# Kernel optimization log

Measured on AMD Instinct MI355X. Metric: run time of the kernel, lower is better.

Reference implementation:

```python
import math
import jax, jax.numpy as jnp
import numpy as np

DIM = 1536; NH = 12; HD = DIM // NH        # head_dim = 128
F, H, W = 4, 20, 26
S = F * H * W                              # 2080 tokens
BLOCK = 128
SPAD = math.ceil(S / BLOCK) * BLOCK        # 2176
EPS = 1e-6
C = HD // 2
SF, SH, SW = C - 2 * (C // 3), C // 3, C // 3   # 22, 21, 21 rotary bands


def _rope_params(max_len, d, theta=10000.0):
    inv = 1.0 / (theta ** (np.arange(0, d, 2, dtype=np.float64) / d))
    return np.outer(np.arange(max_len), inv)   # [max_len, d//2] angles


def _rope(x, freqs, f, h, w):
    # x: [b, s, n, d] with s == f*h*w; freqs: [1024, d//2] angles
    b, s, n, d = x.shape
    ang = jnp.concatenate([
        jnp.broadcast_to(freqs[:f, :SF][:, None, None, :], (f, h, w, SF)),
        jnp.broadcast_to(freqs[:h, SF:SF + SH][None, :, None, :], (f, h, w, SH)),
        jnp.broadcast_to(freqs[:w, SF + SH:C][None, None, :, :], (f, h, w, SW)),
    ], axis=-1).reshape(s, C)
    cos = jnp.cos(ang)[None, :, None, :]
    sin = jnp.sin(ang)[None, :, None, :]
    xr = x.reshape(b, s, n, C, 2)
    x0, x1 = xr[..., 0], xr[..., 1]          # complex mult (x0+ix1)*(cos+isin)
    out = jnp.stack([x0 * cos - x1 * sin, x0 * sin + x1 * cos], axis=-1)
    return out.reshape(b, s, n, d)


def setup_inputs():
    key = jax.random.key(0)
    ks = jax.random.split(key, 6)
    freqs = jnp.asarray(np.concatenate([
        _rope_params(1024, 2 * SF), _rope_params(1024, 2 * SH), _rope_params(1024, 2 * SW)
    ], axis=1), dtype=jnp.float32)           # [1024, 64]
    lin = lambda k: jax.random.normal(k, (DIM, DIM), jnp.float32) * 0.02
    blk = jnp.arange(SPAD) // BLOCK
    # block-causal (128-token blocks) mask, padding keys (>= S) masked out
    mask = (blk[:, None] >= blk[None, :]) & (jnp.arange(SPAD)[None, :] < S)
    return {
        "x": jax.random.normal(ks[0], (1, S, DIM), jnp.float32),
        "freqs": freqs,
        "wq": lin(ks[1]), "bq": jnp.zeros((DIM,), jnp.float32),
        "wk": lin(ks[2]), "bk": jnp.zeros((DIM,), jnp.float32),
        "wv": lin(ks[3]), "bv": jnp.zeros((DIM,), jnp.float32),
        "wo": lin(ks[4]), "bo": jnp.zeros((DIM,), jnp.float32),
        "gq": jnp.ones((DIM,), jnp.float32),
        "gk": jnp.ones((DIM,), jnp.float32),
        "seq_lens": jnp.array([S], jnp.int32),
        "grid_sizes": jnp.array([[F, H, W]], jnp.int32),
        "mask": mask,
    }


def reference(x, freqs, wq, bq, wk, bk, wv, bv, wo, bo, gq, gk, seq_lens, grid_sizes, mask):
    b, s, _ = x.shape
    n, d = NH, HD
    rms = lambda t, g: (t * jax.lax.rsqrt(jnp.mean(t * t, axis=-1, keepdims=True) + EPS)) * g
    q = rms(x @ wq + bq, gq).reshape(b, s, n, d)
    k = rms(x @ wk + bk, gk).reshape(b, s, n, d)
    v = (x @ wv + bv).reshape(b, s, n, d)
    f, h, w = int(grid_sizes[0, 0]), int(grid_sizes[0, 1]), int(grid_sizes[0, 2])
    sl = int(seq_lens[0])
    if sl > 0 and s == 2 * sl:  # teacher forcing: rope each half independently
        q = jnp.concatenate([_rope(q[:, :sl], freqs, f, h, w), _rope(q[:, sl:], freqs, f, h, w)], axis=1)
        k = jnp.concatenate([_rope(k[:, :sl], freqs, f, h, w), _rope(k[:, sl:], freqs, f, h, w)], axis=1)
    else:
        q = _rope(q, freqs, f, h, w)
        k = _rope(k, freqs, f, h, w)
    pad = SPAD - s
    if pad > 0:
        pz = ((0, 0), (0, pad), (0, 0), (0, 0))
        q, k, v = jnp.pad(q, pz), jnp.pad(k, pz), jnp.pad(v, pz)
    scores = jnp.einsum('bqnd,bknd->bnqk', q, k) / math.sqrt(d)
    scores = jnp.where(mask[None, None], scores, -jnp.inf)
    attn = jax.nn.softmax(scores, axis=-1)
    o = jnp.einsum('bnqk,bknd->bqnd', attn, v)[:, :s].reshape(b, s, n * d)
    return o @ wo + bo
```

## Files before the change

### kernel.cpp

```cpp
#include <hip/hip_runtime.h>

#define DIMM   1536
#define NHEAD  12
#define HD     128
#define SEQ    2080
#define SPADN  2176
#define HWPROD 520
#define SCALE  0.08838834764831845f
#define K2F    0.12751744154f

typedef short short8  __attribute__((ext_vector_type(8)));
typedef float floatx4 __attribute__((ext_vector_type(4)));

__device__ __forceinline__ unsigned short f2bf(float f) {
    union { float f; unsigned u; } v; v.f = f;
    return (unsigned short)((v.u + 0x7fffu + ((v.u >> 16) & 1u)) >> 16);
}

__device__ __forceinline__ void gld_lds16(const void* g, void* l) {
    __builtin_amdgcn_global_load_lds(
        (const __attribute__((address_space(1))) unsigned int*)g,
        (__attribute__((address_space(3))) unsigned int*)l, 16, 0, 0);
}

__constant__ int c_base[33] = {0,1,2,3,4,5,6,7,
                               8,10,12,14,16,18,20,22,
                               24,27,30,33,36,39,42,45,
                               48,52,56,60,64,68,72,76,
                               80};
#define SLOTS_PER_HEAD 85

__global__ void k_prep(const float* __restrict__ x,
                       const float* __restrict__ w0, const float* __restrict__ w1,
                       const float* __restrict__ w2, const float* __restrict__ w3,
                       unsigned short* __restrict__ xb,
                       unsigned short* __restrict__ t0, unsigned short* __restrict__ t1,
                       unsigned short* __restrict__ t2, unsigned short* __restrict__ t3) {
    int z = blockIdx.z;
    if (z == 4) {
        int n4 = SEQ * DIMM / 4;
        int idx = (blockIdx.y * 24 + blockIdx.x) * 256 + threadIdx.x;
#pragma unroll
        for (int i = 0; i < 6; i++) {
            int p = idx + i * 147456;
            if (p < n4) {
                float4 v = ((const float4*)x)[p];
                ushort4 o;
                o.x = f2bf(v.x); o.y = f2bf(v.y); o.z = f2bf(v.z); o.w = f2bf(v.w);
                ((ushort4*)xb)[p] = o;
            }
        }
        return;
    }
    const float* in = (z == 0) ? w0 : (z == 1) ? w1 : (z == 2) ? w2 : w3;
    unsigned short* out = (z == 0) ? t0 : (z == 1) ? t1 : (z == 2) ? t2 : t3;
    __shared__ float tile[64][65];
    int tx = threadIdx.x & 63, ty = threadIdx.x >> 6;
    int r0 = blockIdx.x * 64, c0 = blockIdx.y * 64;
#pragma unroll
    for (int i = 0; i < 16; i++)
        tile[i * 4 + ty][tx] = in[(size_t)(r0 + i * 4 + ty) * DIMM + c0 + tx];
    __syncthreads();
#pragma unroll
    for (int i = 0; i < 16; i++) {
        int cc = i * 4 + ty;
        out[(size_t)(c0 + cc) * DIMM + r0 + tx] = f2bf(tile[tx][cc]);
    }
}

__global__ void k_transpose_bf16(const float* __restrict__ in, unsigned short* __restrict__ out,
                                 int Rvalid, int Rout, int C) {
    __shared__ float tile[64][65];
    int tx = threadIdx.x & 63, ty = threadIdx.x >> 6;
    int r0 = blockIdx.x * 64, c0 = blockIdx.y * 64;
#pragma unroll
    for (int i = 0; i < 16; i++) {
        int rr = i * 4 + ty;
        int gr = r0 + rr;
        tile[rr][tx] = (gr < Rvalid) ? in[(size_t)gr * C + c0 + tx] : 0.f;
    }
    __syncthreads();
#pragma unroll
    for (int i = 0; i < 16; i++) {
        int cc = i * 4 + ty;
        out[(size_t)(c0 + cc) * Rout + r0 + tx] = f2bf(tile[tx][cc]);
    }
}

__global__ __launch_bounds__(256, 3) void k_gemm(
    const unsigned short* __restrict__ A,
    const unsigned short* __restrict__ B0, const unsigned short* __restrict__ B1,
    const unsigned short* __restrict__ B2,
    const float* __restrict__ bias0, const float* __restrict__ bias1, const float* __restrict__ bias2,
    float* __restrict__ C0, float* __restrict__ C1, float* __restrict__ C2,
    int M, int N, int K) {
    const unsigned short* B = B0; const float* bias = bias0; float* C = C0;
    if (blockIdx.z == 1) { B = B1; bias = bias1; C = C1; }
    if (blockIdx.z == 2) { B = B2; bias = bias2; C = C2; }

    __shared__ unsigned short As[128 * 64];
    __shared__ unsigned short Bs[128 * 64];

    int tid = threadIdx.x;
    int lane = tid & 63, wv = tid >> 6;
    int quad = lane >> 4, l16 = lane & 15;
    int m0 = blockIdx.y * 128, n0 = blockIdx.x * 128;
    int wm = (wv >> 1) * 64, wn = (wv & 1) * 64;
    int sw = l16 & 7;

    int srow_in_blk = lane >> 3;
    int schunk = lane & 7;
    int gchunk = schunk ^ (srow_in_blk & 7);

    floatx4 acc[4][4];
#pragma unroll
    for (int i = 0; i < 4; i++)
#pragma unroll
        for (int j = 0; j < 4; j++) acc[i][j] = (floatx4){0.f, 0.f, 0.f, 0.f};

    for (int k0 = 0; k0 < K; k0 += 64) {
#pragma unroll
        for (int i = 0; i < 4; i++) {
            int blkrow = (wv * 4 + i) * 8;
            int r = blkrow + srow_in_blk;
            int ra = m0 + r; if (ra > M - 1) ra = M - 1;
            gld_lds16(A + (size_t)ra * K + k0 + gchunk * 8, &As[blkrow * 64]);
            gld_lds16(B + (size_t)(n0 + r) * K + k0 + gchunk * 8, &Bs[blkrow * 64]);
        }
        __syncthreads();
#pragma unroll
        for (int kc = 0; kc < 2; kc++) {
            short8 af[4], bfr[4];
#pragma unroll
            for (int t = 0; t < 4; t++) {
                int ca = ((kc * 4 + quad) ^ sw) << 3;
                af[t]  = *(const short8*)&As[(wm + t * 16 + l16) * 64 + ca];
                bfr[t] = *(const short8*)&Bs[(wn + t * 16 + l16) * 64 + ca];
            }
#pragma unroll
            for (int mi = 0; mi < 4; mi++)
#pragma unroll
                for (int ni = 0; ni < 4; ni++)
                    acc[mi][ni] = __builtin_amdgcn_mfma_f32_16x16x32_bf16(af[mi], bfr[ni], acc[mi][ni], 0, 0, 0);
        }
        __syncthreads();
    }
#pragma unroll
    for (int mi = 0; mi < 4; mi++) {
#pragma unroll
        for (int r = 0; r < 4; r++) {
            int row = m0 + wm + mi * 16 + quad * 4 + r;
            if (row < M) {
#pragma unroll
                for (int ni = 0; ni < 4; ni++) {
                    int col = n0 + wn + ni * 16 + l16;
                    C[(size_t)row * N + col] = acc[mi][ni][r] + bias[col];
                }
            }
        }
    }
}

__global__ __launch_bounds__(256, 8) void k_gemm64(
    const unsigned short* __restrict__ A, const unsigned short* __restrict__ B,
    const float* __restrict__ bias, float* __restrict__ C, int M, int N, int K) {
    __shared__ unsigned short As[64 * 64];
    __shared__ unsigned short Bs[64 * 64];
    int tid = threadIdx.x;
    int lane = tid & 63, wv = tid >> 6;
    int quad = lane >> 4, l16 = lane & 15;
    int m0 = blockIdx.y * 64, n0 = blockIdx.x * 64;
    int wm = (wv >> 1) * 32, wn = (wv & 1) * 32;

    int srow = lane >> 3;
    int schunk = lane & 7;

    floatx4 acc[2][2];
#pragma unroll
    for (int i = 0; i < 2; i++)
#pragma unroll
        for (int j = 0; j < 2; j++) acc[i][j] = (floatx4){0.f, 0.f, 0.f, 0.f};

    for (int k0 = 0; k0 < K; k0 += 64) {
#pragma unroll
        for (int i = 0; i < 2; i++) {
            int rb = (i * 4 + wv) * 8;
            int r = rb + srow;
            int g = schunk ^ (r & 7);
            int ra = m0 + r; if (ra > M - 1) ra = M - 1;
            gld_lds16(A + (size_t)ra * K + k0 + g * 8, &As[rb * 64]);
            gld_lds16(B + (size_t)(n0 + r) * K + k0 + g * 8, &Bs[rb * 64]);
        }
        __syncthreads();
#pragma unroll
        for (int kc = 0; kc < 2; kc++) {
            short8 af[2], bfr[2];
#pragma unroll
            for (int t = 0; t < 2; t++) {
                int rowa = wm + t * 16 + l16;
                int rowb = wn + t * 16 + l16;
                int c = kc * 4 + quad;
                af[t]  = *(const short8*)&As[rowa * 64 + ((c ^ (rowa & 7)) << 3)];
                bfr[t] = *(const short8*)&Bs[rowb * 64 + ((c ^ (rowb & 7)) << 3)];
            }
#pragma unroll
            for (int mi = 0; mi < 2; mi++)
#pragma unroll
                for (int ni = 0; ni < 2; ni++)
                    acc[mi][ni] = __builtin_amdgcn_mfma_f32_16x16x32_bf16(af[mi], bfr[ni], acc[mi][ni], 0, 0, 0);
        }
        __syncthreads();
    }
#pragma unroll
    for (int mi = 0; mi < 2; mi++) {
#pragma unroll
        for (int r = 0; r < 4; r++) {
            int row = m0 + wm + mi * 16 + quad * 4 + r;
            if (row < M) {
#pragma unroll
                for (int ni = 0; ni < 2; ni++) {
                    int col = n0 + wn + ni * 16 + l16;
                    C[(size_t)row * N + col] = acc[mi][ni][r] + bias[col];
                }
            }
        }
    }
}

__global__ void k_rmsrope(const float* __restrict__ Qf, const float* __restrict__ Kf,
                          const float* __restrict__ gq, const float* __restrict__ gk,
                          const float* __restrict__ freqs,
                          unsigned short* __restrict__ Qa, unsigned short* __restrict__ Ka) {
    __shared__ float redq[4], redk[4];
    int s = blockIdx.x;
    int tid = threadIdx.x;
    int lane = tid & 63, wv = tid >> 6;
    const float2* qrow = (const float2*)(Qf + (size_t)s * DIMM);
    const float2* krow = (const float2*)(Kf + (size_t)s * DIMM);
    const float2* g2q = (const float2*)gq;
    const float2* g2k = (const float2*)gk;

    float2 qv[3], kv[3];
    float sq = 0.f, sk = 0.f;
#pragma unroll
    for (int j = 0; j < 3; j++) {
        int p = tid + j * 256;
        qv[j] = qrow[p]; kv[j] = krow[p];
        sq += qv[j].x * qv[j].x + qv[j].y * qv[j].y;
        sk += kv[j].x * kv[j].x + kv[j].y * kv[j].y;
    }
#pragma unroll
    for (int m = 32; m >= 1; m >>= 1) { sq += __shfl_xor(sq, m); sk += __shfl_xor(sk, m); }
    if (lane == 0) { redq[wv] = sq; redk[wv] = sk; }
    __syncthreads();
    float tq = redq[0] + redq[1] + redq[2] + redq[3];
    float tk = redk[0] + redk[1] + redk[2] + redk[3];
    float scq = rsqrtf(tq * (1.f / DIMM) + 1e-6f);
    float sck = rsqrtf(tk * (1.f / DIMM) + 1e-6f);

    int fi = s / HWPROD;
    int rem = s - fi * HWPROD;
    int hi = rem / 26;
    int wi = rem - hi * 26;
#pragma unroll
    for (int j = 0; j < 3; j++) {
        int p = tid + j * 256;
        int c = p & 63;
        int pos = (c < 22) ? fi : ((c < 43) ? hi : wi);
        float ang = freqs[pos * 64 + c];
        float sn, cs;
        __sincosf(ang, &sn, &cs);
        float2 gqa = g2q[p];
        float q0 = qv[j].x * scq * gqa.x, q1 = qv[j].y * scq * gqa.y;
        ushort2 oq; oq.x = f2bf(q0 * cs - q1 * sn); oq.y = f2bf(q0 * sn + q1 * cs);
        float2 gka = g2k[p];
        float kk0 = kv[j].x * sck * gka.x, kk1 = kv[j].y * sck * gka.y;
        ushort2 ok; ok.x = f2bf(kk0 * cs - kk1 * sn); ok.y = f2bf(kk0 * sn + kk1 * cs);
        int h = p >> 6;
        size_t off = ((size_t)h * SPADN + s) * HD + 2 * c;
        *(ushort2*)(Qa + off) = oq;
        *(ushort2*)(Ka + off) = ok;
    }
}

__global__ __launch_bounds__(256, 3) void k_attn1(const unsigned short* __restrict__ Qa,
                                                  const unsigned short* __restrict__ Ka,
                                                  const unsigned short* __restrict__ Vt,
                                                  float* __restrict__ Opart,
                                                  float* __restrict__ Lpart) {
    int j = blockIdx.x, h = blockIdx.y, z = blockIdx.z;
    int nkb = (j >> 1) * 2 + 2;
    if (nkb > 33) nkb = 33;
    int kb0 = z * 8;
    if (kb0 >= nkb) return;
    int kb1 = kb0 + 8; if (kb1 > nkb) kb1 = nkb;

    __shared__ unsigned short Ks[64 * 128];
    __shared__ unsigned short Vs[128 * 64];
    __shared__ unsigned short Ps[4][16][72];

    int tid = threadIdx.x;
    int lane = tid & 63, wv = tid >> 6;
    int quad = lane >> 4, l16 = lane & 15;
    int qrow0 = j * 64 + wv * 16;

    short8 qf[4];
#pragma unroll
    for (int kc = 0; kc < 4; kc++)
        qf[kc] = *(const short8*)(Qa + ((size_t)h * SPADN + qrow0 + l16) * HD + kc * 32 + quad * 8);

    short8 ones8;
#pragma unroll
    for (int i = 0; i < 8; i++) ones8[i] = (short)0x3F80;

    floatx4 of[8], of9;
#pragma unroll
    for (int ni = 0; ni < 8; ni++) of[ni] = (floatx4){0.f, 0.f, 0.f, 0.f};
    of9 = (floatx4){0.f, 0.f, 0.f, 0.f};

    int krow = lane >> 4;
    int kslot = lane & 15;
    int vrow = lane >> 3;
    int vslot = lane & 7;

    for (int kb = kb0; kb < kb1; kb++) {
        const unsigned short* kbase = Ka + (((size_t)h * SPADN + kb * 64) * HD);
#pragma unroll
        for (int i = 0; i < 4; i++) {
            int rb = i * 4 + wv;
            int r = rb * 4 + krow;
            int g = (kslot & 8) | ((kslot & 7) ^ (r & 7));
            gld_lds16(kbase + r * 128 + g * 8, &Ks[rb * 512]);
        }
#pragma unroll
        for (int i = 0; i < 4; i++) {
            int rb = i * 4 + wv;
            int r = rb * 8 + vrow;
            int g = vslot ^ (r & 7);
            gld_lds16(Vt + ((size_t)h * HD + r) * SPADN + kb * 64 + g * 8, &Vs[rb * 512]);
        }
        __syncthreads();

        floatx4 sa[4];
#pragma unroll
        for (int ni = 0; ni < 4; ni++) sa[ni] = (floatx4){0.f, 0.f, 0.f, 0.f};
#pragma unroll
        for (int kc = 0; kc < 4; kc++) {
            int c = kc * 4 + quad;
            short8 kf[4];
#pragma unroll
            for (int ni = 0; ni < 4; ni++) {
                int row = ni * 16 + l16;
                int slot = (c & 8) | ((c & 7) ^ (row & 7));
                kf[ni] = *(const short8*)&Ks[row * 128 + slot * 8];
            }
#pragma unroll
            for (int ni = 0; ni < 4; ni++)
                sa[ni] = __builtin_amdgcn_mfma_f32_16x16x32_bf16(qf[kc], kf[ni], sa[ni], 0, 0, 0);
        }

        bool maskb = (kb == 32);
#pragma unroll
        for (int r = 0; r < 4; r++) {
#pragma unroll
            for (int ni = 0; ni < 4; ni++) {
                float xv = sa[ni][r] * K2F;
                if (maskb && (kb * 64 + ni * 16 + l16 >= SEQ)) xv = -1e30f;
                float p = exp2f(fminf(xv, 36.f));
                Ps[wv][quad * 4 + r][ni * 16 + l16] = f2bf(p);
            }
        }
#pragma unroll
        for (int kc = 0; kc < 2; kc++) {
            int ko = kc * 32 + quad * 8;
            short8 pf = *(const short8*)&Ps[wv][l16][ko];
            int c = kc * 4 + quad;
#pragma unroll
            for (int ni = 0; ni < 8; ni++) {
                int row = ni * 16 + l16;
                short8 vf = *(const short8*)&Vs[row * 64 + ((c ^ (row & 7)) << 3)];
                of[ni] = __builtin_amdgcn_mfma_f32_16x16x32_bf16(pf, vf, of[ni], 0, 0, 0);
            }
            of9 = __builtin_amdgcn_mfma_f32_16x16x32_bf16(pf, ones8, of9, 0, 0, 0);
        }
        __syncthreads();
    }

    int slot = h * SLOTS_PER_HEAD + c_base[j] + z;
    float* Op = Opart + (size_t)slot * 8192;
#pragma unroll
    for (int r = 0; r < 4; r++) {
        int lrow = wv * 16 + quad * 4 + r;
#pragma unroll
        for (int ni = 0; ni < 8; ni++)
            Op[lrow * 128 + ni * 16 + l16] = of[ni][r];
    }
    if (l16 == 0) {
#pragma unroll
        for (int r = 0; r < 4; r++)
            Lpart[slot * 64 + wv * 16 + quad * 4 + r] = of9[r];
    }
}

__global__ void k_attn2(const float* __restrict__ Opart,
                        const float* __restrict__ Lpart,
                        unsigned short* __restrict__ Ob) {
    int j = blockIdx.x, h = blockIdx.y;
    int nkb = (j >> 1) * 2 + 2; if (nkb > 33) nkb = 33;
    int nc = (nkb + 7) >> 3;
    int base = h * SLOTS_PER_HEAD + c_base[j];
    int t = threadIdx.x;
    int r = t >> 2;
    int c0 = (t & 3) * 32;
    int row = j * 64 + r;
    if (row >= SEQ) return;

    float acc[32];
#pragma unroll
    for (int q = 0; q < 32; q++) acc[q] = 0.f;
    float L = 0.f;
    for (int c = 0; c < nc; c++) {
        L += Lpart[(base + c) * 64 + r];
        const float4* op = (const float4*)(Opart + (size_t)(base + c) * 8192 + r * 128 + c0);
#pragma unroll
        for (int q = 0; q < 8; q++) {
            float4 v = op[q];
            acc[q * 4 + 0] += v.x; acc[q * 4 + 1] += v.y;
            acc[q * 4 + 2] += v.z; acc[q * 4 + 3] += v.w;
        }
    }
    float inv = 1.f / L;
    unsigned short* ob = Ob + (size_t)row * DIMM + h * HD + c0;
#pragma unroll
    for (int q = 0; q < 8; q++) {
        ushort4 o;
        o.x = f2bf(acc[q * 4 + 0] * inv); o.y = f2bf(acc[q * 4 + 1] * inv);
        o.z = f2bf(acc[q * 4 + 2] * inv); o.w = f2bf(acc[q * 4 + 3] * inv);
        *(ushort4*)(ob + q * 4) = o;
    }
}

extern "C" void kernel_launch(void* const* d_in, const int* in_sizes, int n_in,
                              void* d_out, int out_size, void* d_ws, size_t ws_size,
                              hipStream_t stream) {
    const float* x     = (const float*)d_in[0];
    const float* freqs = (const float*)d_in[1];
    const float* wq    = (const float*)d_in[2];
    const float* bq    = (const float*)d_in[3];
    const float* wk    = (const float*)d_in[4];
    const float* bk    = (const float*)d_in[5];
    const float* wv    = (const float*)d_in[6];
    const float* bv    = (const float*)d_in[7];
    const float* wo    = (const float*)d_in[8];
    const float* bo    = (const float*)d_in[9];
    const float* gq    = (const float*)d_in[10];
    const float* gk    = (const float*)d_in[11];
    float* out = (float*)d_out;

    char* ws = (char*)d_ws;
    size_t off = 0;
    auto alloc = [&](size_t bytes) -> void* {
        void* p = ws + off;
        off += (bytes + 255) & ~(size_t)255;
        return p;
    };
    unsigned short* xb  = (unsigned short*)alloc((size_t)SEQ * DIMM * 2);
    unsigned short* wqT = (unsigned short*)alloc((size_t)DIMM * DIMM * 2);
    unsigned short* wkT = (unsigned short*)alloc((size_t)DIMM * DIMM * 2);
    unsigned short* wvT = (unsigned short*)alloc((size_t)DIMM * DIMM * 2);
    unsigned short* woT = (unsigned short*)alloc((size_t)DIMM * DIMM * 2);
    float* Qf = (float*)alloc((size_t)SEQ * DIMM * 4);
    float* Kf = (float*)alloc((size_t)SEQ * DIMM * 4);
    float* Vf = (float*)alloc((size_t)SEQ * DIMM * 4);
    unsigned short* Qa = (unsigned short*)alloc((size_t)NHEAD * SPADN * HD * 2);
    unsigned short* Ka = (unsigned short*)alloc((size_t)NHEAD * SPADN * HD * 2);
    unsigned short* Vt = (unsigned short*)alloc((size_t)DIMM * SPADN * 2);
    unsigned short* Ob = (unsigned short*)alloc((size_t)SEQ * DIMM * 2);
    float* Lpart = (float*)alloc((size_t)12 * SLOTS_PER_HEAD * 64 * 4);
    float* Opart = Qf;
    (void)ws_size; (void)in_sizes; (void)n_in; (void)out_size;

    k_prep<<<dim3(24, 24, 5), 256, 0, stream>>>(x, wq, wk, wv, wo, xb, wqT, wkT, wvT, woT);
    k_gemm<<<dim3(12, 17, 3), 256, 0, stream>>>(xb, wqT, wkT, wvT, bq, bk, bv,
                                                Qf, Kf, Vf, SEQ, DIMM, DIMM);
    k_rmsrope<<<SEQ, 256, 0, stream>>>(Qf, Kf, gq, gk, freqs, Qa, Ka);
    k_transpose_bf16<<<dim3(34, 24), 256, 0, stream>>>(Vf, Vt, SEQ, SPADN, DIMM);
    k_attn1<<<dim3(33, 12, 5), 256, 0, stream>>>(Qa, Ka, Vt, Opart, Lpart);
    k_attn2<<<dim3(33, 12), 256, 0, stream>>>(Opart, Lpart, Ob);
    k_gemm64<<<dim3(24, 33), 256, 0, stream>>>(Ob, woT, bo, out, SEQ, DIMM, DIMM);
}
```

Baseline: 249.3 us.

## Emit bf16 QKV from the projection GEMM and write V transposed in its epilogue

The QKV GEMM epilogue now stores Q and K as bf16 instead of fp32, and stores V directly in the transposed bf16 layout the attention kernel reads. This removes the separate V transpose kernel and cuts the write traffic of the GEMM and the read traffic of the RMSNorm/RoPE kernel roughly in half. In exchange, Q and K are rounded to bf16 before RMSNorm, which costs some precision. The padded rows of Vt are no longer explicitly zeroed, which relies on the attention mask and on the workspace contents. The workspace layout is reshuffled, and the attention partials now alias the start of the workspace.

```diff
diff --git a/kernel.cpp b/kernel.cpp
--- a/kernel.cpp
+++ b/kernel.cpp
@@ -15,6 +15,10 @@
 __device__ __forceinline__ unsigned short f2bf(float f) {
     union { float f; unsigned u; } v; v.f = f;
     return (unsigned short)((v.u + 0x7fffu + ((v.u >> 16) & 1u)) >> 16);
+}
+__device__ __forceinline__ float bf2f(unsigned short u) {
+    union { unsigned u; float f; } v; v.u = ((unsigned)u) << 16;
+    return v.f;
 }
 
 __device__ __forceinline__ void gld_lds16(const void* g, void* l) {
@@ -68,35 +72,17 @@
     }
 }
 
-__global__ void k_transpose_bf16(const float* __restrict__ in, unsigned short* __restrict__ out,
-                                 int Rvalid, int Rout, int C) {
-    __shared__ float tile[64][65];
-    int tx = threadIdx.x & 63, ty = threadIdx.x >> 6;
-    int r0 = blockIdx.x * 64, c0 = blockIdx.y * 64;
-#pragma unroll
-    for (int i = 0; i < 16; i++) {
-        int rr = i * 4 + ty;
-        int gr = r0 + rr;
-        tile[rr][tx] = (gr < Rvalid) ? in[(size_t)gr * C + c0 + tx] : 0.f;
-    }
-    __syncthreads();
-#pragma unroll
-    for (int i = 0; i < 16; i++) {
-        int cc = i * 4 + ty;
-        out[(size_t)(c0 + cc) * Rout + r0 + tx] = f2bf(tile[tx][cc]);
-    }
-}
-
 __global__ __launch_bounds__(256, 3) void k_gemm(
     const unsigned short* __restrict__ A,
     const unsigned short* __restrict__ B0, const unsigned short* __restrict__ B1,
     const unsigned short* __restrict__ B2,
     const float* __restrict__ bias0, const float* __restrict__ bias1, const float* __restrict__ bias2,
-    float* __restrict__ C0, float* __restrict__ C1, float* __restrict__ C2,
+    unsigned short* __restrict__ Qh, unsigned short* __restrict__ Kh,
+    unsigned short* __restrict__ Vt,
     int M, int N, int K) {
-    const unsigned short* B = B0; const float* bias = bias0; float* C = C0;
-    if (blockIdx.z == 1) { B = B1; bias = bias1; C = C1; }
-    if (blockIdx.z == 2) { B = B2; bias = bias2; C = C2; }
+    const unsigned short* B = B0; const float* bias = bias0;
+    if (blockIdx.z == 1) { B = B1; bias = bias1; }
+    if (blockIdx.z == 2) { B = B2; bias = bias2; }
 
     __shared__ unsigned short As[128 * 64];
     __shared__ unsigned short Bs[128 * 64];
@@ -145,16 +131,37 @@
         }
         __syncthreads();
     }
-#pragma unroll
-    for (int mi = 0; mi < 4; mi++) {
-#pragma unroll
-        for (int r = 0; r < 4; r++) {
-            int row = m0 + wm + mi * 16 + quad * 4 + r;
-            if (row < M) {
+    if (blockIdx.z == 2) {
+#pragma unroll
+        for (int mi = 0; mi < 4; mi++) {
+            int row0 = m0 + wm + mi * 16 + quad * 4;
+            if (row0 < M) {
 #pragma unroll
                 for (int ni = 0; ni < 4; ni++) {
                     int col = n0 + wn + ni * 16 + l16;
-                    C[(size_t)row * N + col] = acc[mi][ni][r] + bias[col];
+                    float b = bias[col];
+                    ushort4 o;
+                    o.x = f2bf(acc[mi][ni][0] + b);
+                    o.y = f2bf(acc[mi][ni][1] + b);
+                    o.z = f2bf(acc[mi][ni][2] + b);
+                    o.w = f2bf(acc[mi][ni][3] + b);
+                    *(ushort4*)(Vt + (size_t)col * SPADN + row0) = o;
+                }
+            }
+        }
+    } else {
+        unsigned short* O = (blockIdx.z == 0) ? Qh : Kh;
+#pragma unroll
+        for (int mi = 0; mi < 4; mi++) {
+#pragma unroll
+            for (int r = 0; r < 4; r++) {
+                int row = m0 + wm + mi * 16 + quad * 4 + r;
+                if (row < M) {
+#pragma unroll
+                    for (int ni = 0; ni < 4; ni++) {
+                        int col = n0 + wn + ni * 16 + l16;
+                        O[(size_t)row * DIMM + col] = f2bf(acc[mi][ni][r] + bias[col]);
+                    }
                 }
             }
         }
@@ -227,7 +234,7 @@
     }
 }
 
-__global__ void k_rmsrope(const float* __restrict__ Qf, const float* __restrict__ Kf,
+__global__ void k_rmsrope(const unsigned short* __restrict__ Qh, const unsigned short* __restrict__ Kh,
                           const float* __restrict__ gq, const float* __restrict__ gk,
                           const float* __restrict__ freqs,
                           unsigned short* __restrict__ Qa, unsigned short* __restrict__ Ka) {
@@ -235,8 +242,8 @@
     int s = blockIdx.x;
     int tid = threadIdx.x;
     int lane = tid & 63, wv = tid >> 6;
-    const float2* qrow = (const float2*)(Qf + (size_t)s * DIMM);
-    const float2* krow = (const float2*)(Kf + (size_t)s * DIMM);
+    const ushort2* qrow = (const ushort2*)(Qh + (size_t)s * DIMM);
+    const ushort2* krow = (const ushort2*)(Kh + (size_t)s * DIMM);
     const float2* g2q = (const float2*)gq;
     const float2* g2k = (const float2*)gk;
 
@@ -245,7 +252,9 @@
 #pragma unroll
     for (int j = 0; j < 3; j++) {
         int p = tid + j * 256;
-        qv[j] = qrow[p]; kv[j] = krow[p];
+        ushort2 uq = qrow[p], uk = krow[p];
+        qv[j].x = bf2f(uq.x); qv[j].y = bf2f(uq.y);
+        kv[j].x = bf2f(uk.x); kv[j].y = bf2f(uk.y);
         sq += qv[j].x * qv[j].x + qv[j].y * qv[j].y;
         sk += kv[j].x * kv[j].x + kv[j].y * kv[j].y;
     }
@@ -464,27 +473,25 @@
         off += (bytes + 255) & ~(size_t)255;
         return p;
     };
-    unsigned short* xb  = (unsigned short*)alloc((size_t)SEQ * DIMM * 2);
+    unsigned short* xb  = (unsigned short*)alloc((size_t)SPADN * DIMM * 2);
     unsigned short* wqT = (unsigned short*)alloc((size_t)DIMM * DIMM * 2);
     unsigned short* wkT = (unsigned short*)alloc((size_t)DIMM * DIMM * 2);
     unsigned short* wvT = (unsigned short*)alloc((size_t)DIMM * DIMM * 2);
+    unsigned short* Qh  = (unsigned short*)alloc((size_t)SEQ * DIMM * 2);
+    unsigned short* Kh  = (unsigned short*)alloc((size_t)SEQ * DIMM * 2);
     unsigned short* woT = (unsigned short*)alloc((size_t)DIMM * DIMM * 2);
-    float* Qf = (float*)alloc((size_t)SEQ * DIMM * 4);
-    float* Kf = (float*)alloc((size_t)SEQ * DIMM * 4);
-    float* Vf = (float*)alloc((size_t)SEQ * DIMM * 4);
-    unsigned short* Qa = (unsigned short*)alloc((size_t)NHEAD * SPADN * HD * 2);
-    unsigned short* Ka = (unsigned short*)alloc((size_t)NHEAD * SPADN * HD * 2);
-    unsigned short* Vt = (unsigned short*)alloc((size_t)DIMM * SPADN * 2);
-    unsigned short* Ob = (unsigned short*)alloc((size_t)SEQ * DIMM * 2);
+    unsigned short* Qa  = (unsigned short*)alloc((size_t)NHEAD * SPADN * HD * 2);
+    unsigned short* Ka  = (unsigned short*)alloc((size_t)NHEAD * SPADN * HD * 2);
+    unsigned short* Vt  = (unsigned short*)alloc((size_t)DIMM * SPADN * 2);
+    unsigned short* Ob  = (unsigned short*)alloc((size_t)SEQ * DIMM * 2);
     float* Lpart = (float*)alloc((size_t)12 * SLOTS_PER_HEAD * 64 * 4);
-    float* Opart = Qf;
+    float* Opart = (float*)ws;
     (void)ws_size; (void)in_sizes; (void)n_in; (void)out_size;
 
     k_prep<<<dim3(24, 24, 5), 256, 0, stream>>>(x, wq, wk, wv, wo, xb, wqT, wkT, wvT, woT);
     k_gemm<<<dim3(12, 17, 3), 256, 0, stream>>>(xb, wqT, wkT, wvT, bq, bk, bv,
-                                                Qf, Kf, Vf, SEQ, DIMM, DIMM);
-    k_rmsrope<<<SEQ, 256, 0, stream>>>(Qf, Kf, gq, gk, freqs, Qa, Ka);
-    k_transpose_bf16<<<dim3(34, 24), 256, 0, stream>>>(Vf, Vt, SEQ, SPADN, DIMM);
+                                                Qh, Kh, Vt, SEQ, DIMM, DIMM);
+    k_rmsrope<<<SEQ, 256, 0, stream>>>(Qh, Kh, gq, gk, freqs, Qa, Ka);
     k_attn1<<<dim3(33, 12, 5), 256, 0, stream>>>(Qa, Ka, Vt, Opart, Lpart);
     k_attn2<<<dim3(33, 12), 256, 0, stream>>>(Opart, Lpart, Ob);
     k_gemm64<<<dim3(24, 33), 256, 0, stream>>>(Ob, woT, bo, out, SEQ, DIMM, DIMM);
```

Result: faster. 238.0 us (-4.5%).
